# Optimization experiments

Hardware: AMD Instinct MI355X
Metric: run time of the kernel (lower is better)

Reference implementation:

```python
import jax, jax.numpy as jnp
import numpy as np

D = 1024
K = 256
B = 8192


def setup_inputs() -> dict:
    key = jax.random.key(0)
    kx, kw, kd, kp = jax.random.split(key, 4)
    x = jax.random.normal(kx, (B, D), dtype=jnp.float32)
    # scale weights ~1/sqrt(d) so the 11-matmul chain stays numerically sane
    Ws = jax.random.normal(kw, (10, D, D), dtype=jnp.float32) / jnp.sqrt(jnp.float32(D))
    W_dec = jax.random.normal(kd, (D, K), dtype=jnp.float32) / jnp.sqrt(jnp.float32(K))
    perm = jax.random.randint(kp, (K,), 0, D, dtype=jnp.int64)
    return {"x": x, "Ws": Ws, "W_dec": W_dec, "perm": perm}


def reference(x, Ws, W_dec, perm):
    # torch nn.Linear(d,d,bias=False): y = x @ W.T
    # source applies fc1..fc9, then fc9 AGAIN, then fc10 (11 matmuls, 10 weights)
    order = list(range(9)) + [8, 9]
    h = x
    for i in order:
        h = h @ Ws[i].T  # [B, D]
    y = h[:, perm]        # vectorized gather, replaces per-row python loop [B, K]
    out = y @ W_dec.T     # fc_decode: [B, D]
    return out
```

## Files before the change

kernel.cpp:

```cpp
#include <hip/hip_runtime.h>
#include <stdint.h>
#include <stddef.h>

typedef __bf16 bf16;
typedef __bf16 bf16x8 __attribute__((ext_vector_type(8)));
typedef float f32x4 __attribute__((ext_vector_type(4)));

__device__ __forceinline__ void global_to_lds16(const void* g, void* l) {
  const __attribute__((address_space(1))) unsigned* gp =
      reinterpret_cast<const __attribute__((address_space(1))) unsigned*>(
          reinterpret_cast<uintptr_t>(g));
  __attribute__((address_space(3))) unsigned* lp =
      reinterpret_cast<__attribute__((address_space(3))) unsigned*>(
          reinterpret_cast<uintptr_t>(l));
  __builtin_amdgcn_global_load_lds(gp, lp, 16, 0, 0);
}

__device__ __forceinline__ void tile8x8_swizzle(int t, int& bx, int& by) {
  bx = (((t >> 3) & 1) << 2) | (t & 3);
  by = (((t >> 4) & 3) << 1) | ((t >> 2) & 1);
}

template <typename OutT>
__device__ __forceinline__ void gemm128_body(const bf16* __restrict__ A,
                                             const bf16* __restrict__ B,
                                             OutT* __restrict__ C,
                                             int bx, int by) {
  __shared__ bf16 As[2][128 * 64];
  __shared__ bf16 Bs[2][128 * 64];

  const int tid = threadIdx.x;
  const int wave = tid >> 6, lane = tid & 63;
  const int quad = lane >> 4, l16 = lane & 15;
  const int rowBase = by * 128;
  const int colBase = bx * 128;
  const int waveM = (wave >> 1) * 64, waveN = (wave & 1) * 64;

  const int sr = tid >> 2;
  const int sc = (tid & 3) * 8;
  const bf16* Ag0 = A + (size_t)(rowBase + sr) * 1024 + sc;
  const bf16* Ag1 = Ag0 + (size_t)64 * 1024;
  const bf16* Bg0 = B + (size_t)(colBase + sr) * 1024 + sc;
  const bf16* Bg1 = Bg0 + (size_t)64 * 1024;

  const int woff = wave * 1024;

  auto issue = [&](int k0, int p) {
    char* aB = (char*)As[p] + woff;
    char* bB = (char*)Bs[p] + woff;
    global_to_lds16(Ag0 + k0,      aB);
    global_to_lds16(Ag1 + k0,      aB + 4096);
    global_to_lds16(Ag0 + k0 + 32, aB + 8192);
    global_to_lds16(Ag1 + k0 + 32, aB + 12288);
    global_to_lds16(Bg0 + k0,      bB);
    global_to_lds16(Bg1 + k0,      bB + 4096);
    global_to_lds16(Bg0 + k0 + 32, bB + 8192);
    global_to_lds16(Bg1 + k0 + 32, bB + 12288);
  };

  f32x4 acc[4][4] = {};

  issue(0, 0);
  int p = 0;
#pragma unroll 1
  for (int k0 = 0; k0 < 1024; k0 += 64, p ^= 1) {
    __syncthreads();
    if (k0 + 64 < 1024) issue(k0 + 64, p ^ 1);
#pragma unroll
    for (int kk = 0; kk < 2; kk++) {
      const bf16* base = As[p] + kk * 4096;
      const bf16* baseB = Bs[p] + kk * 4096;
      bf16x8 af[4], bfr[4];
#pragma unroll
      for (int mi = 0; mi < 4; mi++)
        af[mi] = *(const bf16x8*)(base + (waveM + mi * 16 + l16) * 32 + quad * 8);
#pragma unroll
      for (int ni = 0; ni < 4; ni++)
        bfr[ni] = *(const bf16x8*)(baseB + (waveN + ni * 16 + l16) * 32 + quad * 8);
#pragma unroll
      for (int mi = 0; mi < 4; mi++)
#pragma unroll
        for (int ni = 0; ni < 4; ni++)
          acc[mi][ni] = __builtin_amdgcn_mfma_f32_16x16x32_bf16(af[mi], bfr[ni],
                                                                acc[mi][ni], 0, 0, 0);
    }
  }

  OutT* Cb = C + (size_t)(rowBase + waveM) * 1024 + colBase + waveN;
#pragma unroll
  for (int mi = 0; mi < 4; mi++)
#pragma unroll
    for (int ni = 0; ni < 4; ni++)
#pragma unroll
      for (int r = 0; r < 4; r++)
        Cb[(size_t)(mi * 16 + quad * 4 + r) * 1024 + ni * 16 + l16] =
            (OutT)acc[mi][ni][r];
}

struct PrepArgs {
  const float* cvt_src[5]; bf16* cvt_dst[5];
  const float* tr_src[6];  bf16* tr_dst[6];
  const float* Wdec; const int* praw; bf16* Gbf;
};

__global__ __launch_bounds__(256) void prep_all(PrepArgs p) {
  __shared__ alignas(16) char smem[64 * 65 * 2];
  const int b = blockIdx.x;
  const int tid = threadIdx.x;

  if (b < 2560) {
    const int m = b >> 9, blk = b & 511;
    const float* __restrict__ src = p.cvt_src[m];
    bf16* __restrict__ dst = p.cvt_dst[m];
    const int i = (blk * 256 + tid) * 8;
    float4 a = *(const float4*)(src + i);
    float4 c = *(const float4*)(src + i + 4);
    bf16x8 o;
    o[0] = (bf16)a.x; o[1] = (bf16)a.y; o[2] = (bf16)a.z; o[3] = (bf16)a.w;
    o[4] = (bf16)c.x; o[5] = (bf16)c.y; o[6] = (bf16)c.z; o[7] = (bf16)c.w;
    *(bf16x8*)(dst + i) = o;
  } else if (b < 4096) {
    const int t = b - 2560;
    const int m = t >> 8, r = t & 255;
    const float* __restrict__ src = p.tr_src[m];
    bf16* __restrict__ dst = p.tr_dst[m];
    bf16(*tile)[65] = reinterpret_cast<bf16(*)[65]>(smem);
    const int bx = (r & 15) * 64;
    const int by = (r >> 4) * 64;
    const int tx = tid & 63;
    const int ty4 = tid >> 6;
#pragma unroll
    for (int rr = 0; rr < 16; rr++) {
      int row = ty4 * 16 + rr;
      tile[row][tx] = (bf16)src[(size_t)(by + row) * 1024 + bx + tx];
    }
    __syncthreads();
#pragma unroll
    for (int rr = 0; rr < 16; rr++) {
      int row = ty4 * 16 + rr;
      dst[(size_t)(bx + row) * 1024 + by + tx] = tile[tx][row];
    }
  } else {
    const int j = b - 4096;
    float* row = (float*)smem;
    int* perm_l = (int*)(smem + 4096);
    int* nzp = (int*)(smem + 4096 + 1024);
#pragma unroll
    for (int c = 0; c < 4; c++) row[tid * 4 + c] = 0.f;
    if (tid == 0) *nzp = 0;
    __syncthreads();
    if (tid < 128 && p.praw[2 * tid + 1] != 0) atomicOr(nzp, 1);
    __syncthreads();
    const int is64 = (*nzp == 0);
    perm_l[tid] = is64 ? p.praw[2 * tid] : p.praw[tid];
    __syncthreads();
    atomicAdd(&row[perm_l[tid]], p.Wdec[(size_t)j * 256 + tid]);
    __syncthreads();
#pragma unroll
    for (int c = 0; c < 4; c++)
      p.Gbf[(size_t)j * 1024 + tid * 4 + c] = (bf16)row[tid * 4 + c];
  }
}

struct TreeArgs {
  const bf16* A[6]; const bf16* B[6]; bf16* C[6];
  int nG;
  const float* x; bf16* xbf; int ubase;
};

__global__ __launch_bounds__(256) void tree_level(TreeArgs a) {
  const int b = blockIdx.x;
  const int gBlocks = a.nG * 64;
  if (b < gBlocks) {
    const int z = b >> 6, t = b & 63;
    int bx, by;
    tile8x8_swizzle(t, bx, by);
    gemm128_body<bf16>(a.A[z], a.B[z], a.C[z], bx, by);
  } else {
    const int unit = a.ubase + (b - gBlocks);
    const int i = unit * 2048 + (int)threadIdx.x * 8;
    float4 v0 = *(const float4*)(a.x + i);
    float4 v1 = *(const float4*)(a.x + i + 4);
    bf16x8 o;
    o[0] = (bf16)v0.x; o[1] = (bf16)v0.y; o[2] = (bf16)v0.z; o[3] = (bf16)v0.w;
    o[4] = (bf16)v1.x; o[5] = (bf16)v1.y; o[6] = (bf16)v1.z; o[7] = (bf16)v1.w;
    *(bf16x8*)(a.xbf + i) = o;
  }
}

__global__ __launch_bounds__(256) void final_gemm(const bf16* __restrict__ A,
                                                  const bf16* __restrict__ B,
                                                  float* __restrict__ C) {
  const int b = blockIdx.x;
  gemm128_body<float>(A, B, C, b >> 6, b & 63);
}

extern "C" void kernel_launch(void* const* d_in, const int* in_sizes, int n_in,
                              void* d_out, int out_size, void* d_ws, size_t ws_size,
                              hipStream_t stream) {
  const float* x    = (const float*)d_in[0];
  const float* Wsrc = (const float*)d_in[1];
  const float* Wdec = (const float*)d_in[2];
  const int*   praw = (const int*)d_in[3];
  float* out = (float*)d_out;

  constexpr size_t MAT  = 1024ull * 1024ull;
  constexpr size_t SLOT = 2ull * 1024 * 1024;

  char* ws = (char*)d_ws;
  bf16* Wrm[5];
  for (int i = 0; i < 5; i++) Wrm[i] = (bf16*)(ws + (size_t)i * SLOT);
  bf16* Wt[6];
  for (int i = 0; i < 6; i++) Wt[i] = (bf16*)(ws + (size_t)(5 + i) * SLOT);
  bf16* Gbf = (bf16*)(ws + 11 * SLOT);
  bf16* xbf = (bf16*)(ws + 12 * SLOT);
  bf16* P[6];
  for (int i = 0; i < 6; i++) P[i] = (bf16*)(ws + (size_t)(20 + i) * SLOT);
  bf16* Q[3];
  for (int i = 0; i < 3; i++) Q[i] = (bf16*)(ws + (size_t)(26 + i) * SLOT);
  bf16* Rb = (bf16*)(ws + 29 * SLOT);
  bf16* Fb = (bf16*)(ws + 30 * SLOT);

  PrepArgs pa;
  const int rmIdx[5] = {1, 3, 5, 7, 8};
  for (int i = 0; i < 5; i++) { pa.cvt_src[i] = Wsrc + (size_t)rmIdx[i] * MAT; pa.cvt_dst[i] = Wrm[i]; }
  const int trIdx[6] = {0, 2, 4, 6, 8, 9};
  for (int i = 0; i < 6; i++) { pa.tr_src[i] = Wsrc + (size_t)trIdx[i] * MAT; pa.tr_dst[i] = Wt[i]; }
  pa.Wdec = Wdec; pa.praw = praw; pa.Gbf = Gbf;
  prep_all<<<dim3(5120), 256, 0, stream>>>(pa);

  TreeArgs L1{};
  const bf16* l1a[6] = {Gbf, Wt[4], Wrm[3], Wt[2], Wrm[1], Wt[0]};
  const bf16* l1b[6] = {Wt[5], Wrm[4], Wt[3], Wrm[2], Wt[1], Wrm[0]};
  for (int i = 0; i < 6; i++) { L1.A[i] = l1a[i]; L1.B[i] = l1b[i]; L1.C[i] = P[i]; }
  L1.nG = 6; L1.x = x; L1.xbf = xbf; L1.ubase = 0;
  tree_level<<<dim3(384), 256, 0, stream>>>(L1);

  TreeArgs L2{};
  const bf16* l2a[3] = {P[0], P[3], P[5]};
  const bf16* l2b[3] = {P[1], P[2], P[4]};
  for (int i = 0; i < 3; i++) { L2.A[i] = l2a[i]; L2.B[i] = l2b[i]; L2.C[i] = Q[i]; }
  L2.nG = 3; L2.x = x; L2.xbf = xbf; L2.ubase = 0;
  tree_level<<<dim3(192 + 1360), 256, 0, stream>>>(L2);

  TreeArgs L3{};
  L3.A[0] = Q[0]; L3.B[0] = Q[1]; L3.C[0] = Rb;
  L3.nG = 1; L3.x = x; L3.xbf = xbf; L3.ubase = 1360;
  tree_level<<<dim3(64 + 1360), 256, 0, stream>>>(L3);

  TreeArgs L4{};
  L4.A[0] = Rb; L4.B[0] = Q[2]; L4.C[0] = Fb;
  L4.nG = 1; L4.x = x; L4.xbf = xbf; L4.ubase = 2720;
  tree_level<<<dim3(64 + 1376), 256, 0, stream>>>(L4);

  final_gemm<<<dim3(512), 256, 0, stream>>>(xbf, Fb, out);

  (void)in_sizes; (void)n_in; (void)out_size; (void)ws_size;
}
```

Measured before the change: 197.1 us.

## Rebalance x conversion across tree levels and use 128x64 tiles for single-GEMM levels

Each conversion block now handles 8 chunks of x instead of one. The bf16 conversion of x is redistributed so some of it overlaps the six-GEMM first level, with less left for the later levels. Levels 3 and 4 each run a single 1024x1024 GEMM, and they now use a new 128x64-tile kernel with 128 blocks instead of 64. This puts more work groups on the machine for those small GEMMs. The cost is less data reuse per tile and a fixed work split that depends on grid sizes.

```diff
diff --git a/kernel.cpp b/kernel.cpp
--- a/kernel.cpp
+++ b/kernel.cpp
@@ -91,6 +91,80 @@
   for (int mi = 0; mi < 4; mi++)
 #pragma unroll
     for (int ni = 0; ni < 4; ni++)
+#pragma unroll
+      for (int r = 0; r < 4; r++)
+        Cb[(size_t)(mi * 16 + quad * 4 + r) * 1024 + ni * 16 + l16] =
+            (OutT)acc[mi][ni][r];
+}
+
+template <typename OutT>
+__device__ __forceinline__ void gemm128x64_body(const bf16* __restrict__ A,
+                                                const bf16* __restrict__ B,
+                                                OutT* __restrict__ C,
+                                                int bx, int by) {
+  __shared__ bf16 As[2][128 * 64];
+  __shared__ bf16 Bs[2][64 * 64];
+
+  const int tid = threadIdx.x;
+  const int wave = tid >> 6, lane = tid & 63;
+  const int quad = lane >> 4, l16 = lane & 15;
+  const int rowBase = by * 128;
+  const int colBase = bx * 64;
+  const int waveM = (wave >> 1) * 64;
+  const int waveN = (wave & 1) * 32;
+
+  const int sr = tid >> 2;
+  const int sc = (tid & 3) * 8;
+  const bf16* Ag0 = A + (size_t)(rowBase + sr) * 1024 + sc;
+  const bf16* Ag1 = Ag0 + (size_t)64 * 1024;
+  const bf16* Bg0 = B + (size_t)(colBase + sr) * 1024 + sc;
+
+  const int woff = wave * 1024;
+
+  auto issue = [&](int k0, int p) {
+    char* aB = (char*)As[p] + woff;
+    char* bB = (char*)Bs[p] + woff;
+    global_to_lds16(Ag0 + k0,      aB);
+    global_to_lds16(Ag1 + k0,      aB + 4096);
+    global_to_lds16(Ag0 + k0 + 32, aB + 8192);
+    global_to_lds16(Ag1 + k0 + 32, aB + 12288);
+    global_to_lds16(Bg0 + k0,      bB);
+    global_to_lds16(Bg0 + k0 + 32, bB + 4096);
+  };
+
+  f32x4 acc[4][2] = {};
+
+  issue(0, 0);
+  int p = 0;
+#pragma unroll 1
+  for (int k0 = 0; k0 < 1024; k0 += 64, p ^= 1) {
+    __syncthreads();
+    if (k0 + 64 < 1024) issue(k0 + 64, p ^ 1);
+#pragma unroll
+    for (int kk = 0; kk < 2; kk++) {
+      const bf16* base = As[p] + kk * 4096;
+      const bf16* baseB = Bs[p] + kk * 2048;
+      bf16x8 af[4], bfr[2];
+#pragma unroll
+      for (int mi = 0; mi < 4; mi++)
+        af[mi] = *(const bf16x8*)(base + (waveM + mi * 16 + l16) * 32 + quad * 8);
+#pragma unroll
+      for (int ni = 0; ni < 2; ni++)
+        bfr[ni] = *(const bf16x8*)(baseB + (waveN + ni * 16 + l16) * 32 + quad * 8);
+#pragma unroll
+      for (int mi = 0; mi < 4; mi++)
+#pragma unroll
+        for (int ni = 0; ni < 2; ni++)
+          acc[mi][ni] = __builtin_amdgcn_mfma_f32_16x16x32_bf16(af[mi], bfr[ni],
+                                                                acc[mi][ni], 0, 0, 0);
+    }
+  }
+
+  OutT* Cb = C + (size_t)(rowBase + waveM) * 1024 + colBase + waveN;
+#pragma unroll
+  for (int mi = 0; mi < 4; mi++)
+#pragma unroll
+    for (int ni = 0; ni < 2; ni++)
 #pragma unroll
       for (int r = 0; r < 4; r++)
         Cb[(size_t)(mi * 16 + quad * 4 + r) * 1024 + ni * 16 + l16] =
@@ -177,14 +251,36 @@
     tile8x8_swizzle(t, bx, by);
     gemm128_body<bf16>(a.A[z], a.B[z], a.C[z], bx, by);
   } else {
-    const int unit = a.ubase + (b - gBlocks);
-    const int i = unit * 2048 + (int)threadIdx.x * 8;
-    float4 v0 = *(const float4*)(a.x + i);
-    float4 v1 = *(const float4*)(a.x + i + 4);
-    bf16x8 o;
-    o[0] = (bf16)v0.x; o[1] = (bf16)v0.y; o[2] = (bf16)v0.z; o[3] = (bf16)v0.w;
-    o[4] = (bf16)v1.x; o[5] = (bf16)v1.y; o[6] = (bf16)v1.z; o[7] = (bf16)v1.w;
-    *(bf16x8*)(a.xbf + i) = o;
+    const int u0 = a.ubase + (b - gBlocks) * 8;
+#pragma unroll
+    for (int u = 0; u < 8; u++) {
+      const int i = (u0 + u) * 2048 + (int)threadIdx.x * 8;
+      float4 v0 = *(const float4*)(a.x + i);
+      float4 v1 = *(const float4*)(a.x + i + 4);
+      bf16x8 o;
+      o[0] = (bf16)v0.x; o[1] = (bf16)v0.y; o[2] = (bf16)v0.z; o[3] = (bf16)v0.w;
+      o[4] = (bf16)v1.x; o[5] = (bf16)v1.y; o[6] = (bf16)v1.z; o[7] = (bf16)v1.w;
+      *(bf16x8*)(a.xbf + i) = o;
+    }
+  }
+}
+
+__global__ __launch_bounds__(256) void tree_level_hn(TreeArgs a) {
+  const int b = blockIdx.x;
+  if (b < 128) {
+    gemm128x64_body<bf16>(a.A[0], a.B[0], a.C[0], b >> 3, b & 7);
+  } else {
+    const int u0 = a.ubase + (b - 128) * 8;
+#pragma unroll
+    for (int u = 0; u < 8; u++) {
+      const int i = (u0 + u) * 2048 + (int)threadIdx.x * 8;
+      float4 v0 = *(const float4*)(a.x + i);
+      float4 v1 = *(const float4*)(a.x + i + 4);
+      bf16x8 o;
+      o[0] = (bf16)v0.x; o[1] = (bf16)v0.y; o[2] = (bf16)v0.z; o[3] = (bf16)v0.w;
+      o[4] = (bf16)v1.x; o[5] = (bf16)v1.y; o[6] = (bf16)v1.z; o[7] = (bf16)v1.w;
+      *(bf16x8*)(a.xbf + i) = o;
+    }
   }
 }
 
@@ -234,24 +330,24 @@
   const bf16* l1b[6] = {Wt[5], Wrm[4], Wt[3], Wrm[2], Wt[1], Wrm[0]};
   for (int i = 0; i < 6; i++) { L1.A[i] = l1a[i]; L1.B[i] = l1b[i]; L1.C[i] = P[i]; }
   L1.nG = 6; L1.x = x; L1.xbf = xbf; L1.ubase = 0;
-  tree_level<<<dim3(384), 256, 0, stream>>>(L1);
+  tree_level<<<dim3(384 + 256), 256, 0, stream>>>(L1);
 
   TreeArgs L2{};
   const bf16* l2a[3] = {P[0], P[3], P[5]};
   const bf16* l2b[3] = {P[1], P[2], P[4]};
   for (int i = 0; i < 3; i++) { L2.A[i] = l2a[i]; L2.B[i] = l2b[i]; L2.C[i] = Q[i]; }
-  L2.nG = 3; L2.x = x; L2.xbf = xbf; L2.ubase = 0;
-  tree_level<<<dim3(192 + 1360), 256, 0, stream>>>(L2);
+  L2.nG = 3; L2.x = x; L2.xbf = xbf; L2.ubase = 2048;
+  tree_level<<<dim3(192 + 128), 256, 0, stream>>>(L2);
 
   TreeArgs L3{};
   L3.A[0] = Q[0]; L3.B[0] = Q[1]; L3.C[0] = Rb;
-  L3.nG = 1; L3.x = x; L3.xbf = xbf; L3.ubase = 1360;
-  tree_level<<<dim3(64 + 1360), 256, 0, stream>>>(L3);
+  L3.nG = 1; L3.x = x; L3.xbf = xbf; L3.ubase = 3072;
+  tree_level_hn<<<dim3(128 + 64), 256, 0, stream>>>(L3);
 
   TreeArgs L4{};
   L4.A[0] = Rb; L4.B[0] = Q[2]; L4.C[0] = Fb;
-  L4.nG = 1; L4.x = x; L4.xbf = xbf; L4.ubase = 2720;
-  tree_level<<<dim3(64 + 1376), 256, 0, stream>>>(L4);
+  L4.nG = 1; L4.x = x; L4.xbf = xbf; L4.ubase = 3584;
+  tree_level_hn<<<dim3(128 + 64), 256, 0, stream>>>(L4);
 
   final_gemm<<<dim3(512), 256, 0, stream>>>(xbf, Fb, out);
 
```

Measured after the change: 193.3 us. 1.02x faster.
